# Kernel optimization log

Hardware: AMD Instinct MI355X
Metric: run time of the kernel (lower is better)

Reference implementation:

```python
import jax, jax.numpy as jnp
import numpy as np

D_MODEL = 1024

def setup_inputs() -> dict:
    key = jax.random.key(0)
    ks = jax.random.split(key, 7)
    x = jax.random.normal(ks[0], (4, 2048, D_MODEL), dtype=jnp.float32)
    s = 1.0 / np.sqrt(D_MODEL)
    Wq = jax.random.uniform(ks[1], (D_MODEL, D_MODEL), jnp.float32, -s, s)
    bq = jax.random.uniform(ks[2], (D_MODEL,), jnp.float32, -s, s)
    Wk = jax.random.uniform(ks[3], (D_MODEL, D_MODEL), jnp.float32, -s, s)
    bk = jax.random.uniform(ks[4], (D_MODEL,), jnp.float32, -s, s)
    Wv = jax.random.uniform(ks[5], (D_MODEL, D_MODEL), jnp.float32, -s, s)
    bv = jax.random.uniform(ks[6], (D_MODEL,), jnp.float32, -s, s)
    return {"x": x, "Wq": Wq, "bq": bq, "Wk": Wk, "bk": bk, "Wv": Wv, "bv": bv}

def reference(x, Wq, bq, Wk, bk, Wv, bv):
    # single-head self-attention: q,k,v are [B, S, D]
    q = x @ Wq + bq
    k = x @ Wk + bk
    v = x @ Wv + bv
    scale = 1.0 / jnp.sqrt(jnp.asarray(D_MODEL, x.dtype))
    scores = jnp.einsum('bsd,btd->bst', q, k) * scale  # [B, S, S]
    attn = jax.nn.softmax(scores, axis=-1)
    return jnp.einsum('bst,btd->bsd', attn, v)
```

## Files before the change

### kernel.cpp

```cpp
#include <hip/hip_runtime.h>
#include <hip/hip_bf16.h>
#include <stdint.h>


typedef __attribute__((ext_vector_type(8))) short short8;
typedef __attribute__((ext_vector_type(4))) float f32x4;

__device__ __forceinline__ unsigned short f2bf(float f) {
  union { float f; uint32_t u; } c; c.f = f;
  uint32_t u = c.u;
  u += 0x7FFFu + ((u >> 16) & 1u);
  return (unsigned short)(u >> 16);
}

__device__ __forceinline__ void gl16(const void* g, void* l) {
  __builtin_amdgcn_global_load_lds(
      (const __attribute__((address_space(1))) unsigned int*)g,
      (__attribute__((address_space(3))) unsigned int*)l, 16, 0, 0);
}

#define FENCE() asm volatile("" ::: "memory")
#define BARRIER() do { FENCE(); __builtin_amdgcn_s_barrier(); FENCE(); } while (0)
#define VMWAIT(n) asm volatile("s_waitcnt vmcnt(" #n ")" ::: "memory")

__global__ __launch_bounds__(256) void k_qkv(
    const short* __restrict__ A, const short* __restrict__ B,
    short* __restrict__ Cb, short* __restrict__ vT,
    const float* __restrict__ b0, const float* __restrict__ b1,
    const float* __restrict__ b2)
{
  const int b = blockIdx.x;
  const int xcd = b & 7, r = b >> 3;
  const int z = r >> 6;
  const int mem = r & 63;
  const int tm = xcd * 8 + (mem >> 3);
  const int tn = mem & 7;

  __shared__ short lds[18432];

  const int tid  = threadIdx.x;
  const int lane = tid & 63;
  const int wid  = tid >> 6;
  const long tileM = (long)tm * 128;
  const long tileN = (long)tn * 128;
  const short* Az = A;
  const short* Bz = B + (long)z * 1048576L;

  const int c0 = tid, c1 = 256 + tid;
  const short* gA0 = Az + (tileM + (c0 >> 2)) * 1024 + (c0 & 3) * 8;
  const short* gA1 = Az + (tileM + (c1 >> 2)) * 1024 + (c1 & 3) * 8;
  const short* gB0 = Bz + (tileN + (c0 >> 2)) * 1024 + (c0 & 3) * 8;
  const short* gB1 = Bz + (tileN + (c1 >> 2)) * 1024 + (c1 & 3) * 8;

  const int fr = lane & 15, quad = lane >> 4;
  const int waveM = (wid >> 1) * 64, waveN = (wid & 1) * 64;

  f32x4 acc[4][4] = {};

  {
    short* base = lds;
    gl16(gA0, base + c0 * 8);
    gl16(gA1, base + c1 * 8);
    gl16(gB0, base + 4096 + c0 * 8);
    gl16(gB1, base + 4096 + c1 * 8);
  }

  for (int t = 0; t < 32; ++t) {
    __syncthreads();
    if (t + 1 < 32) {
      const int kt = (t + 1) << 5;
      short* base = lds + ((t + 1) & 1) * 8192;
      gl16(gA0 + kt, base + c0 * 8);
      gl16(gA1 + kt, base + c1 * 8);
      gl16(gB0 + kt, base + 4096 + c0 * 8);
      gl16(gB1 + kt, base + 4096 + c1 * 8);
    }
    const short* sA = lds + (t & 1) * 8192;
    const short* sB = sA + 4096;
    short8 af[4], bf[4];
#pragma unroll
    for (int i = 0; i < 4; ++i)
      af[i] = *(const short8*)&sA[(waveM + i * 16 + fr) * 32 + quad * 8];
#pragma unroll
    for (int j = 0; j < 4; ++j)
      bf[j] = *(const short8*)&sB[(waveN + j * 16 + fr) * 32 + quad * 8];
#pragma unroll
    for (int i = 0; i < 4; ++i)
#pragma unroll
      for (int j = 0; j < 4; ++j)
        acc[i][j] = __builtin_amdgcn_mfma_f32_16x16x32_bf16(af[i], bf[j],
                                                            acc[i][j], 0, 0, 0);
  }

  if (z == 2) {
    __syncthreads();
    short* scr = lds + wid * 4608;
#pragma unroll
    for (int j = 0; j < 4; ++j) {
      const float bv = b2[tileN + waveN + j * 16 + fr];
#pragma unroll
      for (int i = 0; i < 4; ++i)
#pragma unroll
        for (int r = 0; r < 4; ++r)
          scr[(j * 16 + fr) * 72 + i * 16 + quad * 4 + r] =
              (short)f2bf(acc[i][j][r] + bv);
    }
    const int gb = tm >> 4;
    const long t0 = (long)(tm & 15) * 128 + waveM;
#pragma unroll
    for (int c = 0; c < 8; ++c) {
      const int rr = c * 8 + (lane >> 3);
      const int cc = (lane & 7) * 8;
      short8 v = *(const short8*)&scr[rr * 72 + cc];
      const long gd = tileN + waveN + rr;
      *(short8*)(vT + ((long)gb << 21) + gd * 2048 + t0 + cc) = v;
    }
  } else {
    __syncthreads();
    short* scr = lds + wid * 4608;
    short* C = Cb + (long)z * 8388608L;
    const float* bias = (z == 0) ? b0 : b1;
#pragma unroll
    for (int j = 0; j < 4; ++j) {
      const float bv = bias[tileN + waveN + j * 16 + fr];
#pragma unroll
      for (int i = 0; i < 4; ++i)
#pragma unroll
        for (int r = 0; r < 4; ++r)
          scr[(i * 16 + quad * 4 + r) * 72 + j * 16 + fr] =
              (short)f2bf(acc[i][j][r] + bv);
    }
#pragma unroll
    for (int c = 0; c < 8; ++c) {
      const int row = c * 8 + (lane >> 3);
      const int col = (lane & 7) * 8;
      short8 v = *(const short8*)&scr[row * 72 + col];
      *(short8*)(C + (tileM + waveM + row) * 1024 + tileN + waveN + col) = v;
    }
  }
}

__global__ __launch_bounds__(512, 2) void k_score(
    const short* __restrict__ A, const short* __restrict__ B,
    short* __restrict__ Pp, float scale, float* __restrict__ rowsum)
{
  __shared__ short lds[65536];

  const int b = blockIdx.x;
  const int xcd = b & 7, jb = b >> 3;
  const int p = xcd * 4 + (jb >> 3);
  const int tn = jb & 7;
  const int z = p >> 3, tm = p & 7;

  const int tid = threadIdx.x;
  const int lane = tid & 63;
  const int wid = tid >> 6;
  const int fr = lane & 15, quad = lane >> 4;
  const int wm = wid >> 2, wn = wid & 3;

  const long tileM = (long)tm * 256;
  const long tileN = (long)tn * 256;
  const short* Az = A + (long)z * 2097152L;
  const short* Bz = B + (long)z * 2097152L;

  const int srow = tid >> 3;
  const int sslot = (tid & 7) ^ (srow & 7);
  const short* gA = Az + (tileM + srow) * 1024 + sslot * 8;
  const short* gB = Bz + (tileN + srow) * 1024 + sslot * 8;

  const int frk = fr & 7;
  const int aBase = wm << 13;
  const int bRow  = 16384 + ((wn >> 1) << 13) + ((wn & 1) << 12);
  const int o0 = ((quad ^ frk) << 3) + (fr << 6);
  const int o1 = (((quad + 4) ^ frk) << 3) + (fr << 6);

  f32x4 acc[8][4] = {};

  auto stageA = [&](int tt) {
    const short* s = gA + tt * 64;
    short* d = &lds[(tt & 1) << 15];
    gl16(s,          d + (tid << 3));
    gl16(s + 65536,  d + 4096 + (tid << 3));
    gl16(s + 131072, d + 8192 + (tid << 3));
    gl16(s + 196608, d + 12288 + (tid << 3));
  };
  auto stageBh = [&](int tt, int h) {
    const short* s = gB + tt * 64 + h * 131072;
    short* d = &lds[((tt & 1) << 15) + 16384 + (h << 13)];
    gl16(s,         d + (tid << 3));
    gl16(s + 65536, d + 4096 + (tid << 3));
  };

  stageA(0); stageBh(0, 0); stageBh(0, 1); stageA(1);
  VMWAIT(4);
  BARRIER();

#pragma unroll 1
  for (int t = 0; t < 16; ++t) {
    const int bb = (t & 1) << 15;
    short8 af0[4][2], af1[4][2], bf0[2][2], bf1[2][2];

#pragma unroll
    for (int i = 0; i < 4; ++i) {
      af0[i][0] = *(const short8*)&lds[bb + aBase + (i << 10) + o0];
      af0[i][1] = *(const short8*)&lds[bb + aBase + (i << 10) + o1];
    }
#pragma unroll
    for (int j = 0; j < 2; ++j) {
      bf0[j][0] = *(const short8*)&lds[bb + bRow + (j << 10) + o0];
      bf0[j][1] = *(const short8*)&lds[bb + bRow + (j << 10) + o1];
    }
    if (t + 1 < 16) stageBh(t + 1, 0);
    BARRIER();
    __builtin_amdgcn_s_setprio(1);
#pragma unroll
    for (int i = 0; i < 4; ++i)
#pragma unroll
      for (int j = 0; j < 2; ++j) {
        acc[i][j] = __builtin_amdgcn_mfma_f32_16x16x32_bf16(af0[i][0], bf0[j][0], acc[i][j], 0, 0, 0);
        acc[i][j] = __builtin_amdgcn_mfma_f32_16x16x32_bf16(af0[i][1], bf0[j][1], acc[i][j], 0, 0, 0);
      }
    __builtin_amdgcn_s_setprio(0);
    BARRIER();

#pragma unroll
    for (int i = 0; i < 4; ++i) {
      af1[i][0] = *(const short8*)&lds[bb + aBase + ((i + 4) << 10) + o0];
      af1[i][1] = *(const short8*)&lds[bb + aBase + ((i + 4) << 10) + o1];
    }
    if (t + 1 < 16) stageBh(t + 1, 1);
    BARRIER();
    __builtin_amdgcn_s_setprio(1);
#pragma unroll
    for (int i = 0; i < 4; ++i)
#pragma unroll
      for (int j = 0; j < 2; ++j) {
        acc[i + 4][j] = __builtin_amdgcn_mfma_f32_16x16x32_bf16(af1[i][0], bf0[j][0], acc[i + 4][j], 0, 0, 0);
        acc[i + 4][j] = __builtin_amdgcn_mfma_f32_16x16x32_bf16(af1[i][1], bf0[j][1], acc[i + 4][j], 0, 0, 0);
      }
    __builtin_amdgcn_s_setprio(0);
    BARRIER();

#pragma unroll
    for (int j = 0; j < 2; ++j) {
      bf1[j][0] = *(const short8*)&lds[bb + bRow + ((j + 2) << 10) + o0];
      bf1[j][1] = *(const short8*)&lds[bb + bRow + ((j + 2) << 10) + o1];
    }
    BARRIER();
    __builtin_amdgcn_s_setprio(1);
#pragma unroll
    for (int i = 0; i < 4; ++i)
#pragma unroll
      for (int j = 0; j < 2; ++j) {
        acc[i + 4][j + 2] = __builtin_amdgcn_mfma_f32_16x16x32_bf16(af1[i][0], bf1[j][0], acc[i + 4][j + 2], 0, 0, 0);
        acc[i + 4][j + 2] = __builtin_amdgcn_mfma_f32_16x16x32_bf16(af1[i][1], bf1[j][1], acc[i + 4][j + 2], 0, 0, 0);
      }
    __builtin_amdgcn_s_setprio(0);
    BARRIER();

    if (t + 2 < 16) stageA(t + 2);
    BARRIER();
    __builtin_amdgcn_s_setprio(1);
#pragma unroll
    for (int i = 0; i < 4; ++i)
#pragma unroll
      for (int j = 0; j < 2; ++j) {
        acc[i][j + 2] = __builtin_amdgcn_mfma_f32_16x16x32_bf16(af0[i][0], bf1[j][0], acc[i][j + 2], 0, 0, 0);
        acc[i][j + 2] = __builtin_amdgcn_mfma_f32_16x16x32_bf16(af0[i][1], bf1[j][1], acc[i][j + 2], 0, 0, 0);
      }
    __builtin_amdgcn_s_setprio(0);
    if (t < 14) { VMWAIT(4); } else { VMWAIT(0); }
    BARRIER();
  }

#pragma unroll
  for (int i = 0; i < 8; ++i)
#pragma unroll
    for (int j = 0; j < 4; ++j)
#pragma unroll
      for (int r = 0; r < 4; ++r)
        acc[i][j][r] = exp2f(acc[i][j][r] * scale);

  float* rsz = rowsum + (long)z * 2048 + tileM + wm * 128;
#pragma unroll
  for (int i = 0; i < 8; ++i)
#pragma unroll
    for (int r = 0; r < 4; ++r) {
      float s = acc[i][0][r] + acc[i][1][r] + acc[i][2][r] + acc[i][3][r];
      s += __shfl_xor(s, 1);
      s += __shfl_xor(s, 2);
      s += __shfl_xor(s, 4);
      s += __shfl_xor(s, 8);
      if (fr == 0) atomicAdd(&rsz[i * 16 + quad * 4 + r], s);
    }

  __syncthreads();
  short* C = Pp + (long)z * 4194304L;
  short* scr = &lds[wid * 4608];
#pragma unroll
  for (int pass = 0; pass < 2; ++pass) {
#pragma unroll
    for (int j = 0; j < 4; ++j)
#pragma unroll
      for (int i = 0; i < 4; ++i)
#pragma unroll
        for (int r = 0; r < 4; ++r)
          scr[(i * 16 + quad * 4 + r) * 72 + j * 16 + fr] =
              (short)f2bf(acc[pass * 4 + i][j][r]);
#pragma unroll
    for (int c = 0; c < 8; ++c) {
      const int row = c * 8 + (lane >> 3);
      const int col = (lane & 7) * 8;
      short8 v = *(const short8*)&scr[row * 72 + col];
      *(short8*)(C + (tileM + wm * 128 + pass * 64 + row) * 2048 +
                 tileN + wn * 64 + col) = v;
    }
  }
}

__global__ __launch_bounds__(256) void k_pv(
    const short* __restrict__ A, const short* __restrict__ B,
    float* __restrict__ Cf, float* __restrict__ rowsum)
{
  const int b = blockIdx.x;
  const int s = b & 7, r0_ = b >> 3;
  const int z = r0_ >> 4;
  const int mem = r0_ & 15;
  const int tm = (s >> 1) * 4 + (mem >> 2);
  const int tn = (s & 1) * 4 + (mem & 3);

  __shared__ short lds[18432];

  const int tid  = threadIdx.x;
  const int lane = tid & 63;
  const int wid  = tid >> 6;
  const long tileM = (long)tm * 128;
  const long tileN = (long)tn * 128;
  const short* Az = A + (long)z * 4194304L;
  const short* Bz = B + (long)z * 2097152L;

  const int c0 = tid, c1 = 256 + tid;
  const short* gA0 = Az + (tileM + (c0 >> 2)) * 2048 + (c0 & 3) * 8;
  const short* gA1 = Az + (tileM + (c1 >> 2)) * 2048 + (c1 & 3) * 8;
  const short* gB0 = Bz + (tileN + (c0 >> 2)) * 2048 + (c0 & 3) * 8;
  const short* gB1 = Bz + (tileN + (c1 >> 2)) * 2048 + (c1 & 3) * 8;

  const int fr = lane & 15, quad = lane >> 4;
  const int waveM = (wid >> 1) * 64, waveN = (wid & 1) * 64;

  f32x4 acc[4][4] = {};

  {
    short* base = lds;
    gl16(gA0, base + c0 * 8);
    gl16(gA1, base + c1 * 8);
    gl16(gB0, base + 4096 + c0 * 8);
    gl16(gB1, base + 4096 + c1 * 8);
  }

  for (int t = 0; t < 64; ++t) {
    __syncthreads();
    if (t + 1 < 64) {
      const int kt = (t + 1) << 5;
      short* base = lds + ((t + 1) & 1) * 8192;
      gl16(gA0 + kt, base + c0 * 8);
      gl16(gA1 + kt, base + c1 * 8);
      gl16(gB0 + kt, base + 4096 + c0 * 8);
      gl16(gB1 + kt, base + 4096 + c1 * 8);
    }
    const short* sA = lds + (t & 1) * 8192;
    const short* sB = sA + 4096;
    short8 af[4], bf[4];
#pragma unroll
    for (int i = 0; i < 4; ++i)
      af[i] = *(const short8*)&sA[(waveM + i * 16 + fr) * 32 + quad * 8];
#pragma unroll
    for (int j = 0; j < 4; ++j)
      bf[j] = *(const short8*)&sB[(waveN + j * 16 + fr) * 32 + quad * 8];
#pragma unroll
    for (int i = 0; i < 4; ++i)
#pragma unroll
      for (int j = 0; j < 4; ++j)
        acc[i][j] = __builtin_amdgcn_mfma_f32_16x16x32_bf16(af[i], bf[j],
                                                            acc[i][j], 0, 0, 0);
  }

  float* C = Cf + (long)z * 2097152L;
#pragma unroll
  for (int i = 0; i < 4; ++i)
#pragma unroll
    for (int r = 0; r < 4; ++r) {
      const long gr = tileM + waveM + i * 16 + quad * 4 + r;
      const float rinv = 1.0f / rowsum[(long)z * 2048 + gr];
#pragma unroll
      for (int j = 0; j < 4; ++j)
        C[gr * 1024 + tileN + waveN + j * 16 + fr] = acc[i][j][r] * rinv;
    }
}

__global__ __launch_bounds__(256) void k_prep(
    const float4* __restrict__ x, ushort4* __restrict__ xb,
    const float* __restrict__ Wq, const float* __restrict__ Wk,
    const float* __restrict__ Wv, short* __restrict__ WT,
    float* __restrict__ rs)
{
  __shared__ short tile[32][33];
  const int b = blockIdx.x;
  if (b < 8192) {
    const long i = (long)b * 256 + threadIdx.x;
    float4 v = x[i];
    ushort4 o;
    o.x = f2bf(v.x); o.y = f2bf(v.y); o.z = f2bf(v.z); o.w = f2bf(v.w);
    xb[i] = o;
  } else if (b < 11264) {
    const int idx = b - 8192;
    const int z = idx >> 10, rem = idx & 1023;
    const float* W = (z == 0) ? Wq : ((z == 1) ? Wk : Wv);
    short* d = WT + (long)z * 1024 * 1024;
    const int n0 = (rem & 31) * 32, d0 = (rem >> 5) * 32;
    const int tx = threadIdx.x & 31, ty = threadIdx.x >> 5;
#pragma unroll
    for (int p = 0; p < 4; ++p)
      tile[ty + p * 8][tx] = (short)f2bf(W[(long)(d0 + ty + p * 8) * 1024 + n0 + tx]);
    __syncthreads();
#pragma unroll
    for (int p = 0; p < 4; ++p)
      d[(long)(n0 + ty + p * 8) * 1024 + d0 + tx] = tile[tx][ty + p * 8];
  } else {
#pragma unroll
    for (int p = 0; p < 32; ++p)
      rs[p * 256 + threadIdx.x] = 0.0f;
  }
}

extern "C" void kernel_launch(void* const* d_in, const int* in_sizes, int n_in,
                              void* d_out, int out_size, void* d_ws, size_t ws_size,
                              hipStream_t stream) {
  const float* x  = (const float*)d_in[0];
  const float* Wq = (const float*)d_in[1];
  const float* bq = (const float*)d_in[2];
  const float* Wk = (const float*)d_in[3];
  const float* bk = (const float*)d_in[4];
  const float* Wv = (const float*)d_in[5];
  const float* bv = (const float*)d_in[6];

  char* ws = (char*)d_ws;
  short* xb  = (short*)(ws);
  short* wt  = (short*)(ws + 16777216);
  short* qkv = (short*)(ws + 23068672);
  short* Pp  = (short*)(ws + 73400320);
  float* rs  = (float*)(ws + 106954752);
  short* vT  = qkv + 2L * 8388608;

  k_prep<<<11265, 256, 0, stream>>>((const float4*)x, (ushort4*)xb,
                                    Wq, Wk, Wv, wt, rs);
  k_qkv<<<1536, 256, 0, stream>>>(xb, wt, qkv, vT, bq, bk, bv);
  k_score<<<256, 512, 0, stream>>>(qkv, qkv + 8388608, Pp,
                                   0.03125f * 1.44269504088896f, rs);
  k_pv<<<512, 256, 0, stream>>>(Pp, vT, (float*)d_out, rs);
}
```

Measured before the change: 249.6 us.

## Restructure QKV GEMM into 256x128 tiles with swizzled LDS and pipelined K=64 stages

```diff
diff --git a/kernel.cpp b/kernel.cpp
--- a/kernel.cpp
+++ b/kernel.cpp
@@ -23,81 +23,116 @@
 #define BARRIER() do { FENCE(); __builtin_amdgcn_s_barrier(); FENCE(); } while (0)
 #define VMWAIT(n) asm volatile("s_waitcnt vmcnt(" #n ")" ::: "memory")
 
-__global__ __launch_bounds__(256) void k_qkv(
+__global__ __launch_bounds__(512, 2) void k_qkv(
     const short* __restrict__ A, const short* __restrict__ B,
     short* __restrict__ Cb, short* __restrict__ vT,
     const float* __restrict__ b0, const float* __restrict__ b1,
     const float* __restrict__ b2)
 {
+  __shared__ short lds[49152];
+
   const int b = blockIdx.x;
   const int xcd = b & 7, r = b >> 3;
-  const int z = r >> 6;
-  const int mem = r & 63;
-  const int tm = xcd * 8 + (mem >> 3);
-  const int tn = mem & 7;
-
-  __shared__ short lds[18432];
-
-  const int tid  = threadIdx.x;
+  const int tm = xcd * 4 + r / 24;
+  const int tn_all = r % 24;
+  const int z = tn_all >> 3, tn = tn_all & 7;
+
+  const int tid = threadIdx.x;
   const int lane = tid & 63;
-  const int wid  = tid >> 6;
-  const long tileM = (long)tm * 128;
+  const int wid = tid >> 6;
+  const int fr = lane & 15, quad = lane >> 4, frk = fr & 7;
+  const int wm = wid >> 1, wn = wid & 1;
+
+  const long tileM = (long)tm * 256;
   const long tileN = (long)tn * 128;
   const short* Az = A;
   const short* Bz = B + (long)z * 1048576L;
 
-  const int c0 = tid, c1 = 256 + tid;
-  const short* gA0 = Az + (tileM + (c0 >> 2)) * 1024 + (c0 & 3) * 8;
-  const short* gA1 = Az + (tileM + (c1 >> 2)) * 1024 + (c1 & 3) * 8;
-  const short* gB0 = Bz + (tileN + (c0 >> 2)) * 1024 + (c0 & 3) * 8;
-  const short* gB1 = Bz + (tileN + (c1 >> 2)) * 1024 + (c1 & 3) * 8;
-
-  const int fr = lane & 15, quad = lane >> 4;
-  const int waveM = (wid >> 1) * 64, waveN = (wid & 1) * 64;
+  const int srow = tid >> 3;
+  const int sslot = (tid & 7) ^ (srow & 7);
+  const short* gA = Az + (tileM + srow) * 1024 + sslot * 8;
+  const short* gB = Bz + (tileN + srow) * 1024 + sslot * 8;
+
+  const int aBase = wm << 12;
+  const int bBase = 16384 + (wn << 12);
+  const int o0 = ((quad ^ frk) << 3) + (fr << 6);
+  const int o1 = (((quad + 4) ^ frk) << 3) + (fr << 6);
 
   f32x4 acc[4][4] = {};
 
-  {
-    short* base = lds;
-    gl16(gA0, base + c0 * 8);
-    gl16(gA1, base + c1 * 8);
-    gl16(gB0, base + 4096 + c0 * 8);
-    gl16(gB1, base + 4096 + c1 * 8);
-  }
-
-  for (int t = 0; t < 32; ++t) {
-    __syncthreads();
-    if (t + 1 < 32) {
-      const int kt = (t + 1) << 5;
-      short* base = lds + ((t + 1) & 1) * 8192;
-      gl16(gA0 + kt, base + c0 * 8);
-      gl16(gA1 + kt, base + c1 * 8);
-      gl16(gB0 + kt, base + 4096 + c0 * 8);
-      gl16(gB1 + kt, base + 4096 + c1 * 8);
-    }
-    const short* sA = lds + (t & 1) * 8192;
-    const short* sB = sA + 4096;
-    short8 af[4], bf[4];
-#pragma unroll
-    for (int i = 0; i < 4; ++i)
-      af[i] = *(const short8*)&sA[(waveM + i * 16 + fr) * 32 + quad * 8];
-#pragma unroll
-    for (int j = 0; j < 4; ++j)
-      bf[j] = *(const short8*)&sB[(waveN + j * 16 + fr) * 32 + quad * 8];
-#pragma unroll
-    for (int i = 0; i < 4; ++i)
-#pragma unroll
-      for (int j = 0; j < 4; ++j)
-        acc[i][j] = __builtin_amdgcn_mfma_f32_16x16x32_bf16(af[i], bf[j],
-                                                            acc[i][j], 0, 0, 0);
-  }
-
+  auto stageA = [&](int tt) {
+    const short* s = gA + tt * 64;
+    short* d = &lds[(tt & 1) * 24576];
+    gl16(s,          d + (tid << 3));
+    gl16(s + 65536,  d + 4096 + (tid << 3));
+    gl16(s + 131072, d + 8192 + (tid << 3));
+    gl16(s + 196608, d + 12288 + (tid << 3));
+  };
+  auto stageB = [&](int tt) {
+    const short* s = gB + tt * 64;
+    short* d = &lds[(tt & 1) * 24576 + 16384];
+    gl16(s,         d + (tid << 3));
+    gl16(s + 65536, d + 4096 + (tid << 3));
+  };
+
+  stageA(0); stageB(0); stageA(1);
+  VMWAIT(4);
+  BARRIER();
+
+#pragma unroll 1
+  for (int t = 0; t < 16; ++t) {
+    const int bb = (t & 1) * 24576;
+    short8 af[4][2], bf0[2][2], bf1[2][2];
+
+#pragma unroll
+    for (int i = 0; i < 4; ++i) {
+      af[i][0] = *(const short8*)&lds[bb + aBase + (i << 10) + o0];
+      af[i][1] = *(const short8*)&lds[bb + aBase + (i << 10) + o1];
+    }
+#pragma unroll
+    for (int j = 0; j < 2; ++j) {
+      bf0[j][0] = *(const short8*)&lds[bb + bBase + (j << 10) + o0];
+      bf0[j][1] = *(const short8*)&lds[bb + bBase + (j << 10) + o1];
+    }
+    if (t + 1 < 16) stageB(t + 1);
+    BARRIER();
+    __builtin_amdgcn_s_setprio(1);
+#pragma unroll
+    for (int i = 0; i < 4; ++i)
+#pragma unroll
+      for (int j = 0; j < 2; ++j) {
+        acc[i][j] = __builtin_amdgcn_mfma_f32_16x16x32_bf16(af[i][0], bf0[j][0], acc[i][j], 0, 0, 0);
+        acc[i][j] = __builtin_amdgcn_mfma_f32_16x16x32_bf16(af[i][1], bf0[j][1], acc[i][j], 0, 0, 0);
+      }
+    __builtin_amdgcn_s_setprio(0);
+    BARRIER();
+
+#pragma unroll
+    for (int j = 0; j < 2; ++j) {
+      bf1[j][0] = *(const short8*)&lds[bb + bBase + ((j + 2) << 10) + o0];
+      bf1[j][1] = *(const short8*)&lds[bb + bBase + ((j + 2) << 10) + o1];
+    }
+    if (t + 2 < 16) stageA(t + 2);
+    BARRIER();
+    __builtin_amdgcn_s_setprio(1);
+#pragma unroll
+    for (int i = 0; i < 4; ++i)
+#pragma unroll
+      for (int j = 0; j < 2; ++j) {
+        acc[i][j + 2] = __builtin_amdgcn_mfma_f32_16x16x32_bf16(af[i][0], bf1[j][0], acc[i][j + 2], 0, 0, 0);
+        acc[i][j + 2] = __builtin_amdgcn_mfma_f32_16x16x32_bf16(af[i][1], bf1[j][1], acc[i][j + 2], 0, 0, 0);
+      }
+    __builtin_amdgcn_s_setprio(0);
+    if (t < 14) { VMWAIT(4); } else { VMWAIT(0); }
+    BARRIER();
+  }
+
+  __syncthreads();
+  short* scr = &lds[wid * 4608];
   if (z == 2) {
-    __syncthreads();
-    short* scr = lds + wid * 4608;
 #pragma unroll
     for (int j = 0; j < 4; ++j) {
-      const float bv = b2[tileN + waveN + j * 16 + fr];
+      const float bv = b2[tileN + wn * 64 + j * 16 + fr];
 #pragma unroll
       for (int i = 0; i < 4; ++i)
 #pragma unroll
@@ -105,24 +140,22 @@
           scr[(j * 16 + fr) * 72 + i * 16 + quad * 4 + r] =
               (short)f2bf(acc[i][j][r] + bv);
     }
-    const int gb = tm >> 4;
-    const long t0 = (long)(tm & 15) * 128 + waveM;
+    const int gb = tm >> 3;
+    const long t0 = (long)(tm & 7) * 256 + wm * 64;
 #pragma unroll
     for (int c = 0; c < 8; ++c) {
       const int rr = c * 8 + (lane >> 3);
       const int cc = (lane & 7) * 8;
       short8 v = *(const short8*)&scr[rr * 72 + cc];
-      const long gd = tileN + waveN + rr;
+      const long gd = tileN + wn * 64 + rr;
       *(short8*)(vT + ((long)gb << 21) + gd * 2048 + t0 + cc) = v;
     }
   } else {
-    __syncthreads();
-    short* scr = lds + wid * 4608;
     short* C = Cb + (long)z * 8388608L;
     const float* bias = (z == 0) ? b0 : b1;
 #pragma unroll
     for (int j = 0; j < 4; ++j) {
-      const float bv = bias[tileN + waveN + j * 16 + fr];
+      const float bv = bias[tileN + wn * 64 + j * 16 + fr];
 #pragma unroll
       for (int i = 0; i < 4; ++i)
 #pragma unroll
@@ -135,7 +168,7 @@
       const int row = c * 8 + (lane >> 3);
       const int col = (lane & 7) * 8;
       short8 v = *(const short8*)&scr[row * 72 + col];
-      *(short8*)(C + (tileM + waveM + row) * 1024 + tileN + waveN + col) = v;
+      *(short8*)(C + (tileM + wm * 64 + row) * 1024 + tileN + wn * 64 + col) = v;
     }
   }
 }
@@ -454,7 +487,7 @@
 
   k_prep<<<11265, 256, 0, stream>>>((const float4*)x, (ushort4*)xb,
                                     Wq, Wk, Wv, wt, rs);
-  k_qkv<<<1536, 256, 0, stream>>>(xb, wt, qkv, vT, bq, bk, bv);
+  k_qkv<<<768, 512, 0, stream>>>(xb, wt, qkv, vT, bq, bk, bv);
   k_score<<<256, 512, 0, stream>>>(qkv, qkv + 8388608, Pp,
                                    0.03125f * 1.44269504088896f, rs);
   k_pv<<<512, 256, 0, stream>>>(Pp, vT, (float*)d_out, rs);
```

Result: faster. 243.2 us (median of 2 runs) (-2.6%).
